# Kernel tuning notes

Hardware: AMD Instinct MI355X
Metric: run time of the kernel (lower is better)

Reference implementation:

```python
import jax, jax.numpy as jnp
import numpy as np

LN_EPS = 1e-5
MIN_BW, MAX_BW, BW_FACTOR = 0.1, 10.0, 1.0
BETA = 0.1


def _layernorm(h, g, b):
    mu = jnp.mean(h, axis=-1, keepdims=True)
    var = jnp.mean((h - mu) ** 2, axis=-1, keepdims=True)
    return (h - mu) * jax.lax.rsqrt(var + LN_EPS) * g + b


def _mlp(x, W1, b1, g, beta, W2, b2):
    # Linear -> LayerNorm -> Dropout(eval: identity) -> GELU(exact) -> Linear
    h = x @ W1 + b1
    h = _layernorm(h, g, beta)
    h = jax.nn.gelu(h, approximate=False)
    return h @ W2 + b2


def _normalize(x):
    n = jnp.linalg.norm(x, axis=-1, keepdims=True)
    return x / jnp.maximum(n, 1e-12)


def _bandwidth(x, y):
    # median-heuristic bandwidth on up to 512 samples; no grad through it
    s = min(512, x.shape[0])
    xs, ys = x[:s], y[:s]
    diff = xs[:, None, :] - ys[None, :, :]          # [s, s, K]
    dist_sq = jnp.sum(diff ** 2, axis=-1)
    bw = jnp.sqrt(jnp.median(dist_sq.reshape(-1)) / 2.0) * BW_FACTOR
    return jax.lax.stop_gradient(jnp.clip(bw, MIN_BW, MAX_BW))


def _score_kernel(x, sx, y, sy):
    # 3-term KSD kernel matrix [B, B]
    bw = _bandwidth(x, y)
    bw2 = bw ** 2
    x2 = jnp.sum(x ** 2, axis=-1)
    y2 = jnp.sum(y ** 2, axis=-1)
    dist_sq = jnp.maximum(x2[:, None] + y2[None, :] - 2.0 * (x @ y.T), 0.0)
    k = jnp.exp(-dist_sq / (2.0 * bw2))
    term1 = k * (sx @ sy.T)
    # sum_d (x_i - y_j)_d * sy_jd  = x_i . sy_j - y_j . sy_j
    term2 = (x @ sy.T - jnp.sum(y * sy, axis=-1)[None, :]) * k / bw2
    D = x.shape[-1]
    term3 = dist_sq * k / (bw2 ** 2) - k * D / bw2
    return term1 + term2 + term3


def setup_inputs() -> dict:
    key = jax.random.key(0)
    B, L, D1, H, K = 256, 128, 768, 1024, 256
    ks = jax.random.split(key, 16)

    def w(k, shape):
        return (jax.random.normal(k, shape, dtype=jnp.float32) * 0.02)

    inp = {
        'image_features': jax.random.normal(ks[0], (B, L, D1), dtype=jnp.float32),
        'text_features': jax.random.normal(ks[1], (B, L, D1), dtype=jnp.float32),
        'eps_img': jax.random.normal(ks[2], (B, L, K), dtype=jnp.float32),
        'eps_txt': jax.random.normal(ks[3], (B, L, K), dtype=jnp.float32),
        'attention_mask': jnp.ones((B, L), dtype=jnp.int32),
    }
    # encoders: D1 -> H -> 2K ; score nets: K -> 2K -> K
    for pfx, k1, k2 in (('enc_i', ks[4], ks[5]), ('enc_t', ks[6], ks[7])):
        inp[pfx + '_W1'] = w(k1, (D1, H)); inp[pfx + '_b1'] = jnp.zeros((H,), jnp.float32)
        inp[pfx + '_g'] = jnp.ones((H,), jnp.float32); inp[pfx + '_beta'] = jnp.zeros((H,), jnp.float32)
        inp[pfx + '_W2'] = w(k2, (H, 2 * K)); inp[pfx + '_b2'] = jnp.zeros((2 * K,), jnp.float32)
    for pfx, k1, k2 in (('sc_i', ks[8], ks[9]), ('sc_t', ks[10], ks[11])):
        inp[pfx + '_W1'] = w(k1, (K, 2 * K)); inp[pfx + '_b1'] = jnp.zeros((2 * K,), jnp.float32)
        inp[pfx + '_g'] = jnp.ones((2 * K,), jnp.float32); inp[pfx + '_beta'] = jnp.zeros((2 * K,), jnp.float32)
        inp[pfx + '_W2'] = w(k2, (2 * K, K)); inp[pfx + '_b2'] = jnp.zeros((K,), jnp.float32)
    return inp


def reference(image_features, text_features, attention_mask, eps_img, eps_txt,
              enc_i_W1, enc_i_b1, enc_i_g, enc_i_beta, enc_i_W2, enc_i_b2,
              enc_t_W1, enc_t_b1, enc_t_g, enc_t_beta, enc_t_W2, enc_t_b2,
              sc_i_W1, sc_i_b1, sc_i_g, sc_i_beta, sc_i_W2, sc_i_b2,
              sc_t_W1, sc_t_b1, sc_t_g, sc_t_beta, sc_t_W2, sc_t_b2):
    B = image_features.shape[0]
    img_params = _mlp(image_features, enc_i_W1, enc_i_b1, enc_i_g, enc_i_beta, enc_i_W2, enc_i_b2)
    txt_params = _mlp(text_features, enc_t_W1, enc_t_b1, enc_t_g, enc_t_beta, enc_t_W2, enc_t_b2)
    K = img_params.shape[-1] // 2
    img_mu, img_logvar = img_params[..., :K], img_params[..., K:]
    txt_mu, txt_logvar = txt_params[..., :K], txt_params[..., K:]

    img_z = _normalize(img_mu + eps_img * jnp.exp(0.5 * img_logvar))
    txt_z = _normalize(txt_mu + eps_txt * jnp.exp(0.5 * txt_logvar))

    img_score = _mlp(img_z, sc_i_W1, sc_i_b1, sc_i_g, sc_i_beta, sc_i_W2, sc_i_b2)
    txt_score = _mlp(txt_z, sc_t_W1, sc_t_b1, sc_t_g, sc_t_beta, sc_t_W2, sc_t_b2)

    seq_last = jnp.sum(attention_mask, axis=1).astype(jnp.int32) - 1   # [B]
    bidx = jnp.arange(B)
    xz, yz = img_z[bidx, seq_last], txt_z[bidx, seq_last]
    xs, ys = img_score[bidx, seq_last], txt_score[bidx, seq_last]

    alignment_loss = jnp.mean(_score_kernel(xz, xs, yz, ys))

    kl1 = -0.5 * jnp.sum(1.0 + img_logvar - img_mu ** 2 - jnp.exp(img_logvar), axis=-1)
    kl2 = -0.5 * jnp.sum(1.0 + txt_logvar - txt_mu ** 2 - jnp.exp(txt_logvar), axis=-1)
    kl_loss = (jnp.mean(kl1[bidx, seq_last]) + jnp.mean(kl2[bidx, seq_last])) / 2.0

    total_loss = kl_loss + BETA * alignment_loss
    return total_loss
```

## Files before the change

### kernel.cpp

```cpp
#include <hip/hip_runtime.h>
#include <math.h>

#define Bb   256
#define Lq   128
#define D1   768
#define Hh   1024
#define Kk   256
#define K2v  512

#define OFF_EPSG  0
#define OFF_H1    131072
#define OFF_H2    655360
#define OFF_H3    917504
#define OFF_Z     1179648
#define OFF_SCORE 1310720
#define OFF_DIST  1441792
#define OFF_HIST  1507328
#define OFF_SCAL  1515520
#define OFF_YSY   1515528
#define OFF_BF    1516048

#define UB_XG   0
#define UB_WT   393216
#define WT_EW1I 0
#define WT_EW1T 786432
#define WT_EW2I 1572864
#define WT_EW2T 2097152
#define WT_SW1I 2621440
#define WT_SW1T 2752512
#define WT_SW2I 2883584
#define WT_SW2T 3014656

typedef __attribute__((ext_vector_type(8))) short short8v;
typedef __attribute__((ext_vector_type(4))) float f32x4;

__device__ __forceinline__ float wred(float v){
#pragma unroll
  for (int m = 32; m; m >>= 1) v += __shfl_xor(v, m, 64);
  return v;
}
__device__ __forceinline__ int wredi(int v){
#pragma unroll
  for (int m = 32; m; m >>= 1) v += __shfl_xor(v, m, 64);
  return v;
}
__device__ __forceinline__ float gelu_exact(float x){
  return 0.5f * x * (1.0f + erff(x * 0.70710678118654752f));
}
__device__ __forceinline__ ushort f2b(float f){
  union { float f; unsigned u; } v; v.f = f;
  return (ushort)((v.u + 0x7FFFu + ((v.u >> 16) & 1u)) >> 16);
}
__device__ __forceinline__ int swzq(int k8, int m){
  return ((k8 >> 2)*16 + m)*64 + ((((k8 & 3) << 4)) ^ ((m & 3) << 4));
}
__device__ __forceinline__ int swzr(int ks, int l15, int kg){
  return (ks*16 + l15)*64 + ((kg*16) ^ ((l15 & 3) << 4));
}

__global__ __launch_bounds__(256) void k_prep(
    const float* __restrict__ img, const float* __restrict__ txt,
    const float* __restrict__ epsi, const float* __restrict__ epst,
    const int* __restrict__ mask,
    const float* __restrict__ eW1i, const float* __restrict__ eW1t,
    const float* __restrict__ eW2i, const float* __restrict__ eW2t,
    const float* __restrict__ sW1i, const float* __restrict__ sW1t,
    const float* __restrict__ sW2i, const float* __restrict__ sW2t,
    ushort* __restrict__ xgb, float* __restrict__ epsg, ushort* __restrict__ wt,
    int* __restrict__ ghist, float* __restrict__ scal, float* __restrict__ ysy)
{
  __shared__ float lsf[32][33];
  __shared__ int s_last;
  const int bid = blockIdx.x, t = threadIdx.x;
  if (bid < 256){
    if (t < 8) reinterpret_cast<int4*>(ghist)[bid * 8 + t] = make_int4(0,0,0,0);
    if (bid == 0 && t < 8) scal[t] = 0.0f;
    if (t < 2) ysy[bid * 2 + t] = 0.0f;
    int s = 0;
    if (t < 32){
      int4 v = reinterpret_cast<const int4*>(mask + bid * Lq)[t];
      s = v.x + v.y + v.z + v.w;
    }
    if (t < 64){
      int tot = wredi(s);
      if (t == 0) s_last = tot - 1;
    }
    __syncthreads();
    const int last = s_last;
    if (t < 192){
      float4 v = reinterpret_cast<const float4*>(img + (size_t)(bid*Lq+last)*D1)[t];
      ushort4 o; o.x=f2b(v.x); o.y=f2b(v.y); o.z=f2b(v.z); o.w=f2b(v.w);
      reinterpret_cast<ushort4*>(xgb + (size_t)bid*D1)[t] = o;
      float4 w = reinterpret_cast<const float4*>(txt + (size_t)(bid*Lq+last)*D1)[t];
      ushort4 q; q.x=f2b(w.x); q.y=f2b(w.y); q.z=f2b(w.z); q.w=f2b(w.w);
      reinterpret_cast<ushort4*>(xgb + (size_t)(Bb+bid)*D1)[t] = q;
    }
    if (t < 64){
      reinterpret_cast<float4*>(epsg + (size_t)bid*Kk)[t] =
        reinterpret_cast<const float4*>(epsi + (size_t)(bid*Lq+last)*Kk)[t];
      reinterpret_cast<float4*>(epsg + (size_t)(Bb+bid)*Kk)[t] =
        reinterpret_cast<const float4*>(epst + (size_t)(bid*Lq+last)*Kk)[t];
    }
    return;
  }
  const int wb = bid - 256;
  const float* src; ushort* dst; int Kd, Nd, ti;
  if      (wb < 768){  src=eW1i; dst=wt+WT_EW1I; Kd=768;  Nd=1024; ti=wb; }
  else if (wb < 1536){ src=eW1t; dst=wt+WT_EW1T; Kd=768;  Nd=1024; ti=wb-768; }
  else if (wb < 2048){ src=eW2i; dst=wt+WT_EW2I; Kd=1024; Nd=512;  ti=wb-1536; }
  else if (wb < 2560){ src=eW2t; dst=wt+WT_EW2T; Kd=1024; Nd=512;  ti=wb-2048; }
  else if (wb < 2688){ src=sW1i; dst=wt+WT_SW1I; Kd=256;  Nd=512;  ti=wb-2560; }
  else if (wb < 2816){ src=sW1t; dst=wt+WT_SW1T; Kd=256;  Nd=512;  ti=wb-2688; }
  else if (wb < 2944){ src=sW2i; dst=wt+WT_SW2I; Kd=512;  Nd=256;  ti=wb-2816; }
  else               { src=sW2t; dst=wt+WT_SW2T; Kd=512;  Nd=256;  ti=wb-2944; }
  const int ntile = Nd / 32;
  const int k0 = (ti / ntile) * 32, n0 = (ti % ntile) * 32;
  const int r = t >> 3, q = t & 7;
  float4 v = reinterpret_cast<const float4*>(src + (size_t)(k0+r)*Nd + n0)[q];
  lsf[r][q*4+0]=v.x; lsf[r][q*4+1]=v.y; lsf[r][q*4+2]=v.z; lsf[r][q*4+3]=v.w;
  __syncthreads();
  ushort4 o;
  o.x = f2b(lsf[q*4+0][r]); o.y = f2b(lsf[q*4+1][r]);
  o.z = f2b(lsf[q*4+2][r]); o.w = f2b(lsf[q*4+3][r]);
  *reinterpret_cast<ushort4*>(dst + (size_t)(n0+r)*Kd + k0 + q*4) = o;
}

__global__ __launch_bounds__(256) void k_enc1(
    const ushort* __restrict__ xgb,
    const ushort* __restrict__ WTi, const ushort* __restrict__ WTt,
    const float* __restrict__ b1i, const float* __restrict__ b1t,
    float* __restrict__ H1)
{
  __shared__ __align__(16) char ALS[16 * 768 * 2];
  const int tid = threadIdx.x, lane = tid & 63, w = tid >> 6;
  const int r0 = blockIdx.y * 16, colbase = blockIdx.x * 64;
  const ushort* WT = (r0 >= 256) ? WTt : WTi;
  const float* b1 = (r0 >= 256) ? b1t : b1i;

  for (int q = tid; q < 16 * 96; q += 256){
    int m = q / 96, k8 = q % 96;
    short8v v = *reinterpret_cast<const short8v*>(xgb + (size_t)(r0+m)*D1 + k8*8);
    *reinterpret_cast<short8v*>(ALS + swzq(k8, m)) = v;
  }
  __syncthreads();
  const int l15 = lane & 15, kg = lane >> 4;
  const int col = colbase + w*16 + l15;
  f32x4 acc = (f32x4){0.f,0.f,0.f,0.f};
#pragma unroll 4
  for (int ks = 0; ks < 24; ks++){
    short8v av = *reinterpret_cast<const short8v*>(ALS + swzr(ks, l15, kg));
    short8v bv = *reinterpret_cast<const short8v*>(WT + (size_t)col*D1 + ks*32 + kg*8);
    acc = __builtin_amdgcn_mfma_f32_16x16x32_bf16(av, bv, acc, 0, 0, 0);
  }
  const float bias = b1[col];
#pragma unroll
  for (int r = 0; r < 4; r++)
    H1[(size_t)(r0 + kg*4 + r) * Hh + col] = acc[r] + bias;
}

__global__ __launch_bounds__(512) void k_enc2(
    const float* __restrict__ H1,
    const ushort* __restrict__ WTi, const ushort* __restrict__ WTt,
    const float* __restrict__ gi,  const float* __restrict__ gt,
    const float* __restrict__ bei, const float* __restrict__ bet,
    const float* __restrict__ b2i, const float* __restrict__ b2t,
    float* __restrict__ H2)
{
  __shared__ __align__(16) char ALS[16 * 1024 * 2];
  __shared__ __align__(16) float Rf[4][64][4];
  const int tid = threadIdx.x, lane = tid & 63, w = tid >> 6;
  const int r0 = blockIdx.y * 16, colbase = blockIdx.x * 64;
  const ushort* WT = (r0 >= 256) ? WTt : WTi;
  const float* g  = (r0 >= 256) ? gt  : gi;
  const float* be = (r0 >= 256) ? bet : bei;
  const float* b2 = (r0 >= 256) ? b2t : b2i;

#pragma unroll
  for (int rr = 0; rr < 2; rr++){
    const int row = w + rr*8, grow = r0 + row;
    const float4* h4 = reinterpret_cast<const float4*>(H1 + (size_t)grow * Hh);
    float4 v0 = h4[lane*4+0], v1 = h4[lane*4+1], v2 = h4[lane*4+2], v3 = h4[lane*4+3];
    float s = v0.x+v0.y+v0.z+v0.w + v1.x+v1.y+v1.z+v1.w
            + v2.x+v2.y+v2.z+v2.w + v3.x+v3.y+v3.z+v3.w;
    float q2 = v0.x*v0.x+v0.y*v0.y+v0.z*v0.z+v0.w*v0.w
             + v1.x*v1.x+v1.y*v1.y+v1.z*v1.z+v1.w*v1.w
             + v2.x*v2.x+v2.y*v2.y+v2.z*v2.z+v2.w*v2.w
             + v3.x*v3.x+v3.y*v3.y+v3.z*v3.z+v3.w*v3.w;
    s = wred(s); q2 = wred(q2);
    const float mean = s * (1.0f/1024.0f);
    const float rstd = rsqrtf(q2 * (1.0f/1024.0f) - mean*mean + 1e-5f);
    const float4* g4  = reinterpret_cast<const float4*>(g);
    const float4* be4 = reinterpret_cast<const float4*>(be);
    float hv[16] = {v0.x,v0.y,v0.z,v0.w, v1.x,v1.y,v1.z,v1.w,
                    v2.x,v2.y,v2.z,v2.w, v3.x,v3.y,v3.z,v3.w};
    short8v o0, o1;
#pragma unroll
    for (int j = 0; j < 16; j++){
      float4 gg = g4[lane*4 + (j>>2)];
      float4 bb = be4[lane*4 + (j>>2)];
      const float gs = (j&3)==0?gg.x:((j&3)==1?gg.y:((j&3)==2?gg.z:gg.w));
      const float bs = (j&3)==0?bb.x:((j&3)==1?bb.y:((j&3)==2?bb.z:bb.w));
      float x = gelu_exact((hv[j] - mean)*rstd*gs + bs);
      if (j < 8) o0[j] = (short)f2b(x); else o1[j-8] = (short)f2b(x);
    }
    *reinterpret_cast<short8v*>(ALS + swzq(lane*2,   row)) = o0;
    *reinterpret_cast<short8v*>(ALS + swzq(lane*2+1, row)) = o1;
  }
  __syncthreads();
  const int l15 = lane & 15, kg = lane >> 4;
  const int ct = w & 3, khalf = w >> 2;
  const int col = colbase + ct*16 + l15;
  f32x4 acc = (f32x4){0.f,0.f,0.f,0.f};
#pragma unroll 4
  for (int i = 0; i < 16; i++){
    const int ks = khalf*16 + i;
    short8v av = *reinterpret_cast<const short8v*>(ALS + swzr(ks, l15, kg));
    short8v bv = *reinterpret_cast<const short8v*>(WT + (size_t)col*Hh + ks*32 + kg*8);
    acc = __builtin_amdgcn_mfma_f32_16x16x32_bf16(av, bv, acc, 0, 0, 0);
  }
  if (khalf) *reinterpret_cast<float4*>(&Rf[ct][lane][0]) = make_float4(acc[0],acc[1],acc[2],acc[3]);
  __syncthreads();
  if (!khalf){
    float4 o = *reinterpret_cast<const float4*>(&Rf[ct][lane][0]);
    const float bias = b2[col];
    float r0v = acc[0]+o.x+bias, r1v = acc[1]+o.y+bias, r2v = acc[2]+o.z+bias, r3v = acc[3]+o.w+bias;
    H2[(size_t)(r0 + kg*4 + 0) * K2v + col] = r0v;
    H2[(size_t)(r0 + kg*4 + 1) * K2v + col] = r1v;
    H2[(size_t)(r0 + kg*4 + 2) * K2v + col] = r2v;
    H2[(size_t)(r0 + kg*4 + 3) * K2v + col] = r3v;
  }
}

__global__ __launch_bounds__(256) void k_sc1(
    const float* __restrict__ H2,
    const float* __restrict__ b2i, const float* __restrict__ b2t,
    const float* __restrict__ epsg,
    const ushort* __restrict__ W1i, const ushort* __restrict__ W1t,
    const float* __restrict__ sb1i, const float* __restrict__ sb1t,
    float* __restrict__ z, float* __restrict__ kl, float* __restrict__ H3)
{
  __shared__ __align__(16) char ALS[16 * 256 * 2];
  const int tid = threadIdx.x, lane = tid & 63, w = tid >> 6;
  const int r0 = blockIdx.y * 16, colblk = blockIdx.x, colbase = colblk * 64;
  const float* b2 = (r0 >= 256) ? b2t : b2i;
  const ushort* W1 = (r0 >= 256) ? W1t : W1i;
  const float* sb1 = (r0 >= 256) ? sb1t : sb1i;

#pragma unroll
  for (int rr = 0; rr < 4; rr++){
    const int row = w + rr*4, grow = r0 + row;
    const float4* h4 = reinterpret_cast<const float4*>(H2 + (size_t)grow * K2v);
    float4 mu = h4[lane], lv = h4[64 + lane];
    float4 bm = reinterpret_cast<const float4*>(b2)[lane];
    float4 bl = reinterpret_cast<const float4*>(b2)[64 + lane];
    mu.x += bm.x; mu.y += bm.y; mu.z += bm.z; mu.w += bm.w;
    lv.x += bl.x; lv.y += bl.y; lv.z += bl.z; lv.w += bl.w;
    float4 ev = reinterpret_cast<const float4*>(epsg)[(size_t)grow * 64 + lane];
    float z0 = mu.x + ev.x * expf(0.5f * lv.x);
    float z1 = mu.y + ev.y * expf(0.5f * lv.y);
    float z2 = mu.z + ev.z * expf(0.5f * lv.z);
    float z3 = mu.w + ev.w * expf(0.5f * lv.w);
    float s2 = wred(z0*z0 + z1*z1 + z2*z2 + z3*z3);
    float klp = (1.0f + lv.x - mu.x*mu.x - expf(lv.x))
              + (1.0f + lv.y - mu.y*mu.y - expf(lv.y))
              + (1.0f + lv.z - mu.z*mu.z - expf(lv.z))
              + (1.0f + lv.w - mu.w*mu.w - expf(lv.w));
    float klt = wred(klp);
    float inv = 1.0f / fmaxf(sqrtf(s2), 1e-12f);
    float4 zv = make_float4(z0*inv, z1*inv, z2*inv, z3*inv);
    if (colblk == 0){
      reinterpret_cast<float4*>(z)[(size_t)grow * 64 + lane] = zv;
      if (lane == 0) atomicAdd(kl + (grow >= 256 ? 1 : 0), -0.5f * klt);
    }
    ushort4 o; o.x=f2b(zv.x); o.y=f2b(zv.y); o.z=f2b(zv.z); o.w=f2b(zv.w);
    *reinterpret_cast<ushort4*>(ALS + swzq(lane >> 1, row) + (lane & 1)*8) = o;
  }
  __syncthreads();
  const int l15 = lane & 15, kg = lane >> 4;
  const int col = colbase + w*16 + l15;
  f32x4 acc = (f32x4){0.f,0.f,0.f,0.f};
#pragma unroll
  for (int ks = 0; ks < 8; ks++){
    short8v av = *reinterpret_cast<const short8v*>(ALS + swzr(ks, l15, kg));
    short8v bv = *reinterpret_cast<const short8v*>(W1 + (size_t)col*Kk + ks*32 + kg*8);
    acc = __builtin_amdgcn_mfma_f32_16x16x32_bf16(av, bv, acc, 0, 0, 0);
  }
  const float bias = sb1[col];
#pragma unroll
  for (int r = 0; r < 4; r++)
    H3[(size_t)(r0 + kg*4 + r) * K2v + col] = acc[r] + bias;
}

__global__ __launch_bounds__(256) void k_sc2(
    const float* __restrict__ H3,
    const float* __restrict__ sgi,  const float* __restrict__ sgt,
    const float* __restrict__ sbei, const float* __restrict__ sbet,
    const ushort* __restrict__ W2i, const ushort* __restrict__ W2t,
    const float* __restrict__ sb2i, const float* __restrict__ sb2t,
    const float* __restrict__ z, float* __restrict__ score, float* __restrict__ ysy,
    float* __restrict__ dist, int* __restrict__ ghist)
{
  __shared__ __align__(16) char SM[33792];
  const int bid = blockIdx.x, tid = threadIdx.x;
  if (bid < 128){
    char* ALS = SM;
    const int lane = tid & 63, w = tid >> 6;
    const int r0 = (bid >> 2) * 16, colbase = (bid & 3) * 64;
    const float* g  = (r0 >= 256) ? sgt  : sgi;
    const float* be = (r0 >= 256) ? sbet : sbei;
    const ushort* W2 = (r0 >= 256) ? W2t : W2i;
    const float* b2 = (r0 >= 256) ? sb2t : sb2i;
#pragma unroll
    for (int rr = 0; rr < 4; rr++){
      const int row = w + rr*4, grow = r0 + row;
      const float4* h4 = reinterpret_cast<const float4*>(H3 + (size_t)grow * K2v);
      float4 a = h4[lane*2], b = h4[lane*2+1];
      float s = a.x+a.y+a.z+a.w + b.x+b.y+b.z+b.w;
      float q2 = a.x*a.x+a.y*a.y+a.z*a.z+a.w*a.w + b.x*b.x+b.y*b.y+b.z*b.z+b.w*b.w;
      s = wred(s); q2 = wred(q2);
      const float mean = s * (1.0f/512.0f);
      const float rstd = rsqrtf(q2 * (1.0f/512.0f) - mean*mean + 1e-5f);
      float4 g0 = reinterpret_cast<const float4*>(g)[lane*2];
      float4 g1 = reinterpret_cast<const float4*>(g)[lane*2+1];
      float4 e0 = reinterpret_cast<const float4*>(be)[lane*2];
      float4 e1 = reinterpret_cast<const float4*>(be)[lane*2+1];
      short8v o;
      o[0] = (short)f2b(gelu_exact((a.x-mean)*rstd*g0.x + e0.x));
      o[1] = (short)f2b(gelu_exact((a.y-mean)*rstd*g0.y + e0.y));
      o[2] = (short)f2b(gelu_exact((a.z-mean)*rstd*g0.z + e0.z));
      o[3] = (short)f2b(gelu_exact((a.w-mean)*rstd*g0.w + e0.w));
      o[4] = (short)f2b(gelu_exact((b.x-mean)*rstd*g1.x + e1.x));
      o[5] = (short)f2b(gelu_exact((b.y-mean)*rstd*g1.y + e1.y));
      o[6] = (short)f2b(gelu_exact((b.z-mean)*rstd*g1.z + e1.z));
      o[7] = (short)f2b(gelu_exact((b.w-mean)*rstd*g1.w + e1.w));
      *reinterpret_cast<short8v*>(ALS + swzq(lane, row)) = o;
    }
    __syncthreads();
    const int l15 = lane & 15, kg = lane >> 4;
    const int col = colbase + w*16 + l15;
    f32x4 acc = (f32x4){0.f,0.f,0.f,0.f};
#pragma unroll 4
    for (int ks = 0; ks < 16; ks++){
      short8v av = *reinterpret_cast<const short8v*>(ALS + swzr(ks, l15, kg));
      short8v bv = *reinterpret_cast<const short8v*>(W2 + (size_t)col*K2v + ks*32 + kg*8);
      acc = __builtin_amdgcn_mfma_f32_16x16x32_bf16(av, bv, acc, 0, 0, 0);
    }
    const float bias = b2[col];
    float part[4];
#pragma unroll
    for (int r = 0; r < 4; r++){
      const int grow = r0 + kg*4 + r;
      const float sv = acc[r] + bias;
      score[(size_t)grow * Kk + col] = sv;
      part[r] = z[(size_t)grow * Kk + col] * sv;
    }
#pragma unroll
    for (int m = 1; m < 16; m <<= 1){
#pragma unroll
      for (int r = 0; r < 4; r++) part[r] += __shfl_xor(part[r], m, 64);
    }
    if (l15 == 0){
#pragma unroll
      for (int r = 0; r < 4; r++) atomicAdd(&ysy[r0 + kg*4 + r], part[r]);
    }
    return;
  }
  float* xsh = reinterpret_cast<float*>(SM);
  int* hl = reinterpret_cast<int*>(SM + 1024);
  const int i = bid - 128, j = tid;
  xsh[j] = z[(size_t)i * Kk + j];
  for (int k = j; k < 8192; k += 256) hl[k] = 0;
  __syncthreads();
  const float4* y4 = reinterpret_cast<const float4*>(z + (size_t)Bb * Kk);
  const float4* x4 = reinterpret_cast<const float4*>(xsh);
  float acc = 0.0f;
#pragma unroll 4
  for (int d = 0; d < Kk; d += 4){
    float4 xv = x4[d >> 2];
    float4 yv = y4[j * (Kk/4) + (d >> 2)];
    float d0 = xv.x - yv.x, d1 = xv.y - yv.y, d2 = xv.z - yv.z, d3 = xv.w - yv.w;
    acc += d0*d0 + d1*d1 + d2*d2 + d3*d3;
  }
  dist[i * 256 + j] = acc;
  int bin = (int)(acc * 2048.0f);
  bin = bin < 0 ? 0 : (bin > 8191 ? 8191 : bin);
  atomicAdd(&hl[bin], 1);
  __syncthreads();
  for (int k = j; k < 8192; k += 256){
    int c = hl[k];
    if (c) atomicAdd(ghist + k, c);
  }
}

__global__ __launch_bounds__(256) void k_score(
    const float* __restrict__ z, const float* __restrict__ score,
    const float* __restrict__ dist, const float* __restrict__ ysy,
    const int* __restrict__ ghist, float* __restrict__ scal,
    float* __restrict__ out)
{
  __shared__ __align__(16) float xsh[Kk];
  __shared__ __align__(16) float sxsh[Kk];
  __shared__ int wt4[4];
  __shared__ int bres[2];
  __shared__ float red4[4];
  __shared__ float s_bw2;
  const int i = blockIdx.x, j = threadIdx.x;
  xsh[j]  = z[(size_t)i * Kk + j];
  sxsh[j] = score[(size_t)i * Kk + j];
  {
    const int lane = j & 63, w = j >> 6;
    const int base = j * 32;
    int s = 0;
#pragma unroll
    for (int u = 0; u < 32; u++) s += ghist[base + u];
    int sc = s;
#pragma unroll
    for (int m = 1; m < 64; m <<= 1){
      int o = __shfl_up(sc, m, 64);
      if (lane >= m) sc += o;
    }
    if (lane == 63) wt4[w] = sc;
    __syncthreads();
    int off = 0;
    for (int q = 0; q < w; q++) off += wt4[q];
    int cum = sc + off, basex = cum - s;
#pragma unroll
    for (int rr = 0; rr < 2; rr++){
      int rank = 32768 + rr;
      if (basex < rank && cum >= rank){
        int c = basex;
        for (int u = 0; u < 32; u++){
          c += ghist[base + u];
          if (c >= rank){ bres[rr] = base + u; break; }
        }
      }
    }
    __syncthreads();
    if (j == 0){
      float med = 0.5f * ((bres[0] + 0.5f) + (bres[1] + 0.5f)) * (1.0f / 2048.0f);
      float bw = sqrtf(med * 0.5f);
      bw = fminf(fmaxf(bw, 0.1f), 10.0f);
      s_bw2 = bw * bw;
    }
    __syncthreads();
  }
  const float bw2 = s_bw2;
  const float4* sy4 = reinterpret_cast<const float4*>(score + (size_t)Bb * Kk);
  const float4* x4  = reinterpret_cast<const float4*>(xsh);
  const float4* sx4 = reinterpret_cast<const float4*>(sxsh);
  float ssy = 0, xsy = 0;
#pragma unroll 4
  for (int d = 0; d < Kk; d += 4){
    float4 xv  = x4[d >> 2];
    float4 sxv = sx4[d >> 2];
    float4 syv = sy4[j * (Kk/4) + (d >> 2)];
    ssy += sxv.x*syv.x + sxv.y*syv.y + sxv.z*syv.z + sxv.w*syv.w;
    xsy += xv.x*syv.x + xv.y*syv.y + xv.z*syv.z + xv.w*syv.w;
  }
  float d2 = dist[i * 256 + j];
  float kv = expf(-d2 / (2.0f * bw2));
  float t1 = kv * ssy;
  float t2 = (xsy - ysy[Bb + j]) * kv / bw2;
  float t3 = d2 * kv / (bw2 * bw2) - kv * (float)Kk / bw2;
  float s = wred(t1 + t2 + t3);
  if (!(j & 63)) red4[j >> 6] = s;
  __syncthreads();
  if (j == 0){
    atomicAdd(scal + 2, red4[0] + red4[1] + red4[2] + red4[3]);
    __threadfence();
    int old = atomicAdd(reinterpret_cast<int*>(scal + 4), 1);
    if (old == 255){
      float kli = __int_as_float(atomicAdd(reinterpret_cast<int*>(scal + 0), 0));
      float klt = __int_as_float(atomicAdd(reinterpret_cast<int*>(scal + 1), 0));
      float alg = __int_as_float(atomicAdd(reinterpret_cast<int*>(scal + 2), 0));
      out[0] = 0.5f * (kli + klt) * (1.0f/256.0f) + 0.1f * alg * (1.0f/65536.0f);
    }
  }
}

extern "C" void kernel_launch(void* const* d_in, const int* in_sizes, int n_in,
                              void* d_out, int out_size, void* d_ws, size_t ws_size,
                              hipStream_t stream) {
  (void)in_sizes; (void)n_in; (void)out_size; (void)ws_size;
  const float* img  = (const float*)d_in[0];
  const float* txt  = (const float*)d_in[1];
  const float* epsi = (const float*)d_in[2];
  const float* epst = (const float*)d_in[3];
  const int*   mask = (const int*)d_in[4];
  const float* eW1i = (const float*)d_in[5];
  const float* eb1i = (const float*)d_in[6];
  const float* egi  = (const float*)d_in[7];
  const float* ebei = (const float*)d_in[8];
  const float* eW2i = (const float*)d_in[9];
  const float* eb2i = (const float*)d_in[10];
  const float* eW1t = (const float*)d_in[11];
  const float* eb1t = (const float*)d_in[12];
  const float* egt  = (const float*)d_in[13];
  const float* ebet = (const float*)d_in[14];
  const float* eW2t = (const float*)d_in[15];
  const float* eb2t = (const float*)d_in[16];
  const float* sW1i = (const float*)d_in[17];
  const float* sb1i = (const float*)d_in[18];
  const float* sgi  = (const float*)d_in[19];
  const float* sbei = (const float*)d_in[20];
  const float* sW2i = (const float*)d_in[21];
  const float* sb2i = (const float*)d_in[22];
  const float* sW1t = (const float*)d_in[23];
  const float* sb1t = (const float*)d_in[24];
  const float* sgt  = (const float*)d_in[25];
  const float* sbet = (const float*)d_in[26];
  const float* sW2t = (const float*)d_in[27];
  const float* sb2t = (const float*)d_in[28];

  float*  ws    = (float*)d_ws;
  float*  epsg  = ws + OFF_EPSG;
  float*  H1    = ws + OFF_H1;
  float*  H2    = ws + OFF_H2;
  float*  H3    = ws + OFF_H3;
  float*  z     = ws + OFF_Z;
  float*  score = ws + OFF_SCORE;
  float*  dist  = ws + OFF_DIST;
  int*    ghist = (int*)(ws + OFF_HIST);
  float*  scal  = ws + OFF_SCAL;
  float*  ysy   = ws + OFF_YSY;
  ushort* ub    = (ushort*)(ws + OFF_BF);
  ushort* xgb   = ub + UB_XG;
  ushort* wt    = ub + UB_WT;

  k_prep<<<3328, 256, 0, stream>>>(img, txt, epsi, epst, mask,
                                   eW1i, eW1t, eW2i, eW2t,
                                   sW1i, sW1t, sW2i, sW2t,
                                   xgb, epsg, wt, ghist, scal, ysy);
  k_enc1<<<dim3(16, 32), 256, 0, stream>>>(xgb, wt+WT_EW1I, wt+WT_EW1T, eb1i, eb1t, H1);
  k_enc2<<<dim3(8, 32), 512, 0, stream>>>(H1, wt+WT_EW2I, wt+WT_EW2T,
                                          egi, egt, ebei, ebet, eb2i, eb2t, H2);
  k_sc1<<<dim3(8, 32), 256, 0, stream>>>(H2, eb2i, eb2t, epsg,
                                         wt+WT_SW1I, wt+WT_SW1T, sb1i, sb1t,
                                         z, scal, H3);
  k_sc2<<<384, 256, 0, stream>>>(H3, sgi, sgt, sbei, sbet,
                                 wt+WT_SW2I, wt+WT_SW2T, sb2i, sb2t,
                                 z, score, ysy, dist, ghist);
  k_score<<<256, 256, 0, stream>>>(z, score, dist, ysy, ghist, scal, (float*)d_out);
}
```

Measured before the change: 87.48 us.

## Spread weight bf16 conversion across later kernels with 64x64 transpose tiles

Weight transpose-to-bf16 conversion is no longer done entirely in the prep kernel. The encoder-2 weights are now converted by extra blocks in the enc1 launch, and the score-net weights by extra blocks in the enc2 launch, so that conversion overlaps with the GEMM work. The transpose tile grows from 32x32 to 64x64, with wider 16-byte stores and fewer blocks. This shortens the prep kernel's critical path, but the conversion blocks now share the GPU with the GEMM blocks, and each conversion block uses more LDS and does more work.

```diff
diff --git a/kernel.cpp b/kernel.cpp
--- a/kernel.cpp
+++ b/kernel.cpp
@@ -58,18 +58,42 @@
   return (ks*16 + l15)*64 + ((kg*16) ^ ((l15 & 3) << 4));
 }
 
+__device__ __forceinline__ void wconv64(
+    const float* __restrict__ src, ushort* __restrict__ dst,
+    int Kd, int Nd, int ti, int t, float (*lsf)[65])
+{
+  const int ntile = Nd >> 6;
+  const int k0 = (ti / ntile) << 6, n0 = (ti % ntile) << 6;
+  const int r = t >> 2, c4 = t & 3;
+  const float4* s4 = reinterpret_cast<const float4*>(src + (size_t)(k0 + r) * Nd + n0);
+#pragma unroll
+  for (int j = 0; j < 4; j++){
+    float4 v = s4[c4 * 4 + j];
+    lsf[r][c4*16 + j*4 + 0] = v.x;
+    lsf[r][c4*16 + j*4 + 1] = v.y;
+    lsf[r][c4*16 + j*4 + 2] = v.z;
+    lsf[r][c4*16 + j*4 + 3] = v.w;
+  }
+  __syncthreads();
+  ushort* d = dst + (size_t)(n0 + r) * Kd + k0 + c4 * 16;
+#pragma unroll
+  for (int h = 0; h < 2; h++){
+    short8v o;
+#pragma unroll
+    for (int j = 0; j < 8; j++) o[j] = (short)f2b(lsf[c4*16 + h*8 + j][r]);
+    *reinterpret_cast<short8v*>(d + h*8) = o;
+  }
+}
+
 __global__ __launch_bounds__(256) void k_prep(
     const float* __restrict__ img, const float* __restrict__ txt,
     const float* __restrict__ epsi, const float* __restrict__ epst,
     const int* __restrict__ mask,
     const float* __restrict__ eW1i, const float* __restrict__ eW1t,
-    const float* __restrict__ eW2i, const float* __restrict__ eW2t,
-    const float* __restrict__ sW1i, const float* __restrict__ sW1t,
-    const float* __restrict__ sW2i, const float* __restrict__ sW2t,
     ushort* __restrict__ xgb, float* __restrict__ epsg, ushort* __restrict__ wt,
     int* __restrict__ ghist, float* __restrict__ scal, float* __restrict__ ysy)
 {
-  __shared__ float lsf[32][33];
+  __shared__ __align__(16) float lsf[64][65];
   __shared__ int s_last;
   const int bid = blockIdx.x, t = threadIdx.x;
   if (bid < 256){
@@ -104,36 +128,29 @@
     return;
   }
   const int wb = bid - 256;
-  const float* src; ushort* dst; int Kd, Nd, ti;
-  if      (wb < 768){  src=eW1i; dst=wt+WT_EW1I; Kd=768;  Nd=1024; ti=wb; }
-  else if (wb < 1536){ src=eW1t; dst=wt+WT_EW1T; Kd=768;  Nd=1024; ti=wb-768; }
-  else if (wb < 2048){ src=eW2i; dst=wt+WT_EW2I; Kd=1024; Nd=512;  ti=wb-1536; }
-  else if (wb < 2560){ src=eW2t; dst=wt+WT_EW2T; Kd=1024; Nd=512;  ti=wb-2048; }
-  else if (wb < 2688){ src=sW1i; dst=wt+WT_SW1I; Kd=256;  Nd=512;  ti=wb-2560; }
-  else if (wb < 2816){ src=sW1t; dst=wt+WT_SW1T; Kd=256;  Nd=512;  ti=wb-2688; }
-  else if (wb < 2944){ src=sW2i; dst=wt+WT_SW2I; Kd=512;  Nd=256;  ti=wb-2816; }
-  else               { src=sW2t; dst=wt+WT_SW2T; Kd=512;  Nd=256;  ti=wb-2944; }
-  const int ntile = Nd / 32;
-  const int k0 = (ti / ntile) * 32, n0 = (ti % ntile) * 32;
-  const int r = t >> 3, q = t & 7;
-  float4 v = reinterpret_cast<const float4*>(src + (size_t)(k0+r)*Nd + n0)[q];
-  lsf[r][q*4+0]=v.x; lsf[r][q*4+1]=v.y; lsf[r][q*4+2]=v.z; lsf[r][q*4+3]=v.w;
-  __syncthreads();
-  ushort4 o;
-  o.x = f2b(lsf[q*4+0][r]); o.y = f2b(lsf[q*4+1][r]);
-  o.z = f2b(lsf[q*4+2][r]); o.w = f2b(lsf[q*4+3][r]);
-  *reinterpret_cast<ushort4*>(dst + (size_t)(n0+r)*Kd + k0 + q*4) = o;
+  if (wb < 192) wconv64(eW1i, wt + WT_EW1I, D1, Hh, wb, t, lsf);
+  else          wconv64(eW1t, wt + WT_EW1T, D1, Hh, wb - 192, t, lsf);
 }
 
 __global__ __launch_bounds__(256) void k_enc1(
     const ushort* __restrict__ xgb,
     const ushort* __restrict__ WTi, const ushort* __restrict__ WTt,
     const float* __restrict__ b1i, const float* __restrict__ b1t,
-    float* __restrict__ H1)
-{
-  __shared__ __align__(16) char ALS[16 * 768 * 2];
-  const int tid = threadIdx.x, lane = tid & 63, w = tid >> 6;
-  const int r0 = blockIdx.y * 16, colbase = blockIdx.x * 64;
+    const float* __restrict__ eW2i, const float* __restrict__ eW2t,
+    ushort* __restrict__ wt, float* __restrict__ H1)
+{
+  __shared__ __align__(16) char SM[16 * 768 * 2];
+  const int bid = blockIdx.x, tid = threadIdx.x;
+  if (bid >= 512){
+    float (*lsf)[65] = reinterpret_cast<float(*)[65]>(SM);
+    const int wb = bid - 512;
+    if (wb < 128) wconv64(eW2i, wt + WT_EW2I, Hh, K2v, wb, tid, lsf);
+    else          wconv64(eW2t, wt + WT_EW2T, Hh, K2v, wb - 128, tid, lsf);
+    return;
+  }
+  char* ALS = SM;
+  const int lane = tid & 63, w = tid >> 6;
+  const int r0 = (bid >> 4) * 16, colbase = (bid & 15) * 64;
   const ushort* WT = (r0 >= 256) ? WTt : WTi;
   const float* b1 = (r0 >= 256) ? b1t : b1i;
 
@@ -164,12 +181,27 @@
     const float* __restrict__ gi,  const float* __restrict__ gt,
     const float* __restrict__ bei, const float* __restrict__ bet,
     const float* __restrict__ b2i, const float* __restrict__ b2t,
-    float* __restrict__ H2)
-{
-  __shared__ __align__(16) char ALS[16 * 1024 * 2];
+    const float* __restrict__ sW1i, const float* __restrict__ sW1t,
+    const float* __restrict__ sW2i, const float* __restrict__ sW2t,
+    ushort* __restrict__ wt, float* __restrict__ H2)
+{
+  __shared__ __align__(16) char SM[16 * 1024 * 2];
   __shared__ __align__(16) float Rf[4][64][4];
-  const int tid = threadIdx.x, lane = tid & 63, w = tid >> 6;
-  const int r0 = blockIdx.y * 16, colbase = blockIdx.x * 64;
+  const int bid = blockIdx.x, tid = threadIdx.x;
+  if (bid >= 256){
+    if (tid < 256){
+      float (*lsf)[65] = reinterpret_cast<float(*)[65]>(SM);
+      const int wb = bid - 256;
+      if      (wb < 32)  wconv64(sW1i, wt + WT_SW1I, Kk,  K2v, wb,      tid, lsf);
+      else if (wb < 64)  wconv64(sW1t, wt + WT_SW1T, Kk,  K2v, wb - 32, tid, lsf);
+      else if (wb < 96)  wconv64(sW2i, wt + WT_SW2I, K2v, Kk,  wb - 64, tid, lsf);
+      else               wconv64(sW2t, wt + WT_SW2T, K2v, Kk,  wb - 96, tid, lsf);
+    }
+    return;
+  }
+  char* ALS = SM;
+  const int lane = tid & 63, w = tid >> 6;
+  const int r0 = (bid >> 3) * 16, colbase = (bid & 7) * 64;
   const ushort* WT = (r0 >= 256) ? WTt : WTi;
   const float* g  = (r0 >= 256) ? gt  : gi;
   const float* be = (r0 >= 256) ? bet : bei;
@@ -223,11 +255,10 @@
   if (!khalf){
     float4 o = *reinterpret_cast<const float4*>(&Rf[ct][lane][0]);
     const float bias = b2[col];
-    float r0v = acc[0]+o.x+bias, r1v = acc[1]+o.y+bias, r2v = acc[2]+o.z+bias, r3v = acc[3]+o.w+bias;
-    H2[(size_t)(r0 + kg*4 + 0) * K2v + col] = r0v;
-    H2[(size_t)(r0 + kg*4 + 1) * K2v + col] = r1v;
-    H2[(size_t)(r0 + kg*4 + 2) * K2v + col] = r2v;
-    H2[(size_t)(r0 + kg*4 + 3) * K2v + col] = r3v;
+    H2[(size_t)(r0 + kg*4 + 0) * K2v + col] = acc[0]+o.x+bias;
+    H2[(size_t)(r0 + kg*4 + 1) * K2v + col] = acc[1]+o.y+bias;
+    H2[(size_t)(r0 + kg*4 + 2) * K2v + col] = acc[2]+o.z+bias;
+    H2[(size_t)(r0 + kg*4 + 3) * K2v + col] = acc[3]+o.w+bias;
   }
 }
 
@@ -527,13 +558,13 @@
   ushort* xgb   = ub + UB_XG;
   ushort* wt    = ub + UB_WT;
 
-  k_prep<<<3328, 256, 0, stream>>>(img, txt, epsi, epst, mask,
-                                   eW1i, eW1t, eW2i, eW2t,
-                                   sW1i, sW1t, sW2i, sW2t,
-                                   xgb, epsg, wt, ghist, scal, ysy);
-  k_enc1<<<dim3(16, 32), 256, 0, stream>>>(xgb, wt+WT_EW1I, wt+WT_EW1T, eb1i, eb1t, H1);
-  k_enc2<<<dim3(8, 32), 512, 0, stream>>>(H1, wt+WT_EW2I, wt+WT_EW2T,
-                                          egi, egt, ebei, ebet, eb2i, eb2t, H2);
+  k_prep<<<640, 256, 0, stream>>>(img, txt, epsi, epst, mask,
+                                  eW1i, eW1t, xgb, epsg, wt, ghist, scal, ysy);
+  k_enc1<<<768, 256, 0, stream>>>(xgb, wt+WT_EW1I, wt+WT_EW1T, eb1i, eb1t,
+                                  eW2i, eW2t, wt, H1);
+  k_enc2<<<384, 512, 0, stream>>>(H1, wt+WT_EW2I, wt+WT_EW2T,
+                                  egi, egt, ebei, ebet, eb2i, eb2t,
+                                  sW1i, sW1t, sW2i, sW2t, wt, H2);
   k_sc1<<<dim3(8, 32), 256, 0, stream>>>(H2, eb2i, eb2t, epsg,
                                          wt+WT_SW1I, wt+WT_SW1T, sb1i, sb1t,
                                          z, scal, H3);
```

New measurement: 88.42 us. About the same (+1.1%).
